# Kernel optimization log

Measured on AMD Instinct MI355X. Metric: run time of the kernel, lower is better.

## Reference

```python
import jax, jax.numpy as jnp
import numpy as np

TEMPERATURE = 0.07
EPS = 1e-12  # matches F.normalize eps

def _l2norm(x, axis):
    n = jnp.sqrt(jnp.sum(x * x, axis=axis, keepdims=True))
    return x / jnp.maximum(n, EPS)

def setup_inputs() -> dict:
    key = jax.random.key(0)
    features = jax.random.normal(key, (512, 256), dtype=jnp.float32)
    return {"features": features}

def reference(features) -> jnp.ndarray:
    B = features.shape[0]
    f = _l2norm(features, axis=1)                      # [B, D]
    fi = f[:, None, :]                                 # broadcast over j
    fj = f[None, :, :]                                 # broadcast over i
    mutual = fi * fj                                   # [B, B, D]
    gate_i = fi * mutual
    gate_j = fj * mutual
    # torch broadcasting: + features adds f[j, k] along trailing dims
    feats_self_i = _l2norm(fi * gate_i + f, axis=2)
    feats_other_i = _l2norm(fi * gate_j + f, axis=2)
    feats_other_j = _l2norm(fj * gate_i + f, axis=2)
    # note: features_self_j is computed in the original but never used in any dot product

    raw_self_i = jnp.einsum('ik,ijk->ij', f, feats_self_i) / TEMPERATURE
    raw_self_j = jnp.einsum('ik,ijk->ij', f, feats_other_j) / TEMPERATURE  # (original uses other_j here)
    raw_other_i = jnp.einsum('ik,ijk->ij', f, feats_other_i) / TEMPERATURE
    raw_other_j = jnp.einsum('ik,ijk->ij', f, feats_other_j) / TEMPERATURE

    logits_mask = 1.0 - jnp.eye(B, dtype=f.dtype)      # zero out diagonal
    exp_sum = (jnp.exp(raw_self_i) + jnp.exp(raw_self_j)
               + jnp.exp(raw_other_i) + jnp.exp(raw_other_j)) * logits_mask
    vs_all = jnp.sum(exp_sum, axis=1, keepdims=True)   # [B, 1]

    log_prob = raw_self_i - jnp.log(vs_all)            # [B, B]
    mean_log_prob_pos = jnp.sum(log_prob, axis=1) / B
    loss = -jnp.mean(mean_log_prob_pos)
    return loss
```

## Files before the change

### kernel.cpp

```cpp
#include <hip/hip_runtime.h>
#include <math.h>

#define Bq 512
#define Dq 256
#define RPB 16
#define PBLK (Bq / RPB)

__device__ __forceinline__ float waveReduceSum(float v) {
    #pragma unroll
    for (int off = 32; off > 0; off >>= 1)
        v += __shfl_xor(v, off, 64);
    return v;
}

__global__ __launch_bounds__(256) void prep_kernel(
        const float* __restrict__ feat,
        float* __restrict__ fT, float* __restrict__ A1,
        float* __restrict__ A2, float* __restrict__ C0,
        float* __restrict__ acc, unsigned int* __restrict__ cnt) {
    const int t = threadIdx.x;
    const int r0 = blockIdx.x * RPB;
    __shared__ float sm[RPB][Dq + 1];
    __shared__ float wpart[RPB][4];
    __shared__ float sinv[RPB];

    float x[RPB];
    #pragma unroll
    for (int r = 0; r < RPB; ++r) x[r] = feat[(r0 + r) * Dq + t];

    const int wid = t >> 6, lane = t & 63;
    #pragma unroll
    for (int r = 0; r < RPB; ++r) {
        float ss = waveReduceSum(x[r] * x[r]);
        if (lane == 0) wpart[r][wid] = ss;
    }
    __syncthreads();
    if (t < RPB) {
        float tot = wpart[t][0] + wpart[t][1] + wpart[t][2] + wpart[t][3];
        sinv[t] = 1.0f / fmaxf(sqrtf(tot), 1e-12f);
    }
    __syncthreads();

    #pragma unroll
    for (int r = 0; r < RPB; ++r) {
        float a  = x[r] * sinv[r];
        float a2 = a * a;
        float c0 = 1.0f + a2 * a;
        A1[(r0 + r) * Dq + t] = a;
        A2[(r0 + r) * Dq + t] = a2;
        C0[(r0 + r) * Dq + t] = c0;
        sm[r][t] = a;
    }
    __syncthreads();

    const int rr = t & 15, kb = t >> 4;
    #pragma unroll
    for (int p = 0; p < 16; ++p) {
        int k = p * 16 + kb;
        fT[k * Bq + r0 + rr] = sm[rr][k];
    }

    if (blockIdx.x == 0 && t == 0) { *acc = 0.0f; *cnt = 0u; }
}

__global__ __launch_bounds__(256) void pair_kernel(
        const float* __restrict__ fT,
        const float* __restrict__ A1, const float* __restrict__ A2,
        const float* __restrict__ C0,
        float* __restrict__ acc, unsigned int* __restrict__ cnt,
        float* __restrict__ out) {
    const int i = blockIdx.x;
    const int t = threadIdx.x;
    const int j0 = 2 * t;

    __shared__ __align__(16) float s_a[Dq];
    __shared__ __align__(16) float s_a2[Dq];
    __shared__ __align__(16) float s_c0[Dq];
    s_a[t]  = A1[i * Dq + t];
    s_a2[t] = A2[i * Dq + t];
    s_c0[t] = C0[i * Dq + t];
    __syncthreads();

    const float4* __restrict__ va  = (const float4*)s_a;
    const float4* __restrict__ va2 = (const float4*)s_a2;
    const float4* __restrict__ vc0 = (const float4*)s_c0;
    const float* __restrict__ pb = fT + j0;

    float du0 = 0.f, nu0 = 0.f, dv0 = 0.f, nv0 = 0.f;
    float du1 = 0.f, nu1 = 0.f, dv1 = 0.f, nv1 = 0.f;

    #pragma unroll 4
    for (int k4 = 0; k4 < Dq / 4; ++k4) {
        float4 a4  = va[k4];
        float4 q4  = va2[k4];
        float4 c4  = vc0[k4];
        const float aa[4] = {a4.x, a4.y, a4.z, a4.w};
        const float qq[4] = {q4.x, q4.y, q4.z, q4.w};
        const float cc[4] = {c4.x, c4.y, c4.z, c4.w};
        #pragma unroll
        for (int kk = 0; kk < 4; ++kk) {
            int k = k4 * 4 + kk;
            float2 bv = *(const float2*)(pb + k * Bq);
            {
                float b  = bv.x;
                float bb = b * b;
                float g  = cc[kk] * b;
                float wb = fmaf(qq[kk], bb, b);
                du0 = fmaf(aa[kk], g,  du0);
                nu0 = fmaf(g,      g,  nu0);
                dv0 = fmaf(aa[kk], wb, dv0);
                nv0 = fmaf(wb,     wb, nv0);
            }
            {
                float b  = bv.y;
                float bb = b * b;
                float g  = cc[kk] * b;
                float wb = fmaf(qq[kk], bb, b);
                du1 = fmaf(aa[kk], g,  du1);
                nu1 = fmaf(g,      g,  nu1);
                dv1 = fmaf(aa[kk], wb, dv1);
                nv1 = fmaf(wb,     wb, nv1);
            }
        }
    }

    const float Tinv = 1.0f / 0.07f;
    float raw_s0 = du0 / fmaxf(sqrtf(nu0), 1e-12f) * Tinv;
    float raw_o0 = dv0 / fmaxf(sqrtf(nv0), 1e-12f) * Tinv;
    float raw_s1 = du1 / fmaxf(sqrtf(nu1), 1e-12f) * Tinv;
    float raw_o1 = dv1 / fmaxf(sqrtf(nv1), 1e-12f) * Tinv;

    float sS = raw_s0 + raw_s1;
    float sV = 0.f;
    if (j0 != i)     sV += expf(raw_s0) + 3.0f * expf(raw_o0);
    if (j0 + 1 != i) sV += expf(raw_s1) + 3.0f * expf(raw_o1);

    sS = waveReduceSum(sS);
    sV = waveReduceSum(sV);
    __shared__ float redS[4], redV[4];
    const int wid = t >> 6, lane = t & 63;
    if (lane == 0) { redS[wid] = sS; redV[wid] = sV; }
    __syncthreads();
    if (t == 0) {
        float S = redS[0] + redS[1] + redS[2] + redS[3];
        float V = redV[0] + redV[1] + redV[2] + redV[3];
        float ti = S * (1.0f / Bq) - logf(V);
        atomicAdd(acc, ti);
        __threadfence();
        unsigned int old = atomicAdd(cnt, 1u);
        if (old == Bq - 1) {
            float tot = atomicAdd(acc, 0.0f);
            out[0] = -tot / (float)Bq;
        }
    }
}

extern "C" void kernel_launch(void* const* d_in, const int* in_sizes, int n_in,
                              void* d_out, int out_size, void* d_ws, size_t ws_size,
                              hipStream_t stream) {
    const float* feat = (const float*)d_in[0];
    float* ws = (float*)d_ws;
    float* fT = ws;
    float* A1 = fT + (size_t)Bq * Dq;
    float* A2 = A1 + (size_t)Bq * Dq;
    float* C0 = A2 + (size_t)Bq * Dq;
    float* acc = C0 + (size_t)Bq * Dq;
    unsigned int* cnt = (unsigned int*)(acc + 1);

    prep_kernel<<<PBLK, 256, 0, stream>>>(feat, fT, A1, A2, C0, acc, cnt);
    pair_kernel<<<Bq, 256, 0, stream>>>(fT, A1, A2, C0, acc, cnt, (float*)d_out);
}
```

Baseline: 91.19 us.

## Tile pair kernel as 2 rows by 256 columns and replace atomics with final reduce

Each pair block now handles two i rows against a 256-wide half of j, so each loaded fT element is reused for two rows instead of loading a float2 for one row. Row normalization and the per-row constants are recomputed inside the pair kernel, which drops the A1/A2/C0 global buffers from the prep kernel. The atomic accumulate with its completion counter is replaced by per-block partial sums written to workspace and a third single-block kernel that does the final reduction. This adds a kernel launch and redundant normalization work per block in exchange for less global traffic and no atomics.

```diff
diff --git a/kernel.cpp b/kernel.cpp
--- a/kernel.cpp
+++ b/kernel.cpp
@@ -14,10 +14,7 @@
 }
 
 __global__ __launch_bounds__(256) void prep_kernel(
-        const float* __restrict__ feat,
-        float* __restrict__ fT, float* __restrict__ A1,
-        float* __restrict__ A2, float* __restrict__ C0,
-        float* __restrict__ acc, unsigned int* __restrict__ cnt) {
+        const float* __restrict__ feat, float* __restrict__ fT) {
     const int t = threadIdx.x;
     const int r0 = blockIdx.x * RPB;
     __shared__ float sm[RPB][Dq + 1];
@@ -40,17 +37,8 @@
         sinv[t] = 1.0f / fmaxf(sqrtf(tot), 1e-12f);
     }
     __syncthreads();
-
     #pragma unroll
-    for (int r = 0; r < RPB; ++r) {
-        float a  = x[r] * sinv[r];
-        float a2 = a * a;
-        float c0 = 1.0f + a2 * a;
-        A1[(r0 + r) * Dq + t] = a;
-        A2[(r0 + r) * Dq + t] = a2;
-        C0[(r0 + r) * Dq + t] = c0;
-        sm[r][t] = a;
-    }
+    for (int r = 0; r < RPB; ++r) sm[r][t] = x[r] * sinv[r];
     __syncthreads();
 
     const int rr = t & 15, kb = t >> 4;
@@ -59,67 +47,75 @@
         int k = p * 16 + kb;
         fT[k * Bq + r0 + rr] = sm[rr][k];
     }
-
-    if (blockIdx.x == 0 && t == 0) { *acc = 0.0f; *cnt = 0u; }
 }
 
 __global__ __launch_bounds__(256) void pair_kernel(
-        const float* __restrict__ fT,
-        const float* __restrict__ A1, const float* __restrict__ A2,
-        const float* __restrict__ C0,
-        float* __restrict__ acc, unsigned int* __restrict__ cnt,
-        float* __restrict__ out) {
-    const int i = blockIdx.x;
+        const float* __restrict__ feat, const float* __restrict__ fT,
+        float* __restrict__ Sp, float* __restrict__ Vp) {
+    const int p = blockIdx.x >> 1;
+    const int h = blockIdx.x & 1;
+    const int i0 = p * 2;
     const int t = threadIdx.x;
-    const int j0 = 2 * t;
+    const int j = h * 256 + t;
+    const int wid = t >> 6, lane = t & 63;
 
-    __shared__ __align__(16) float s_a[Dq];
-    __shared__ __align__(16) float s_a2[Dq];
-    __shared__ __align__(16) float s_c0[Dq];
-    s_a[t]  = A1[i * Dq + t];
-    s_a2[t] = A2[i * Dq + t];
-    s_c0[t] = C0[i * Dq + t];
+    __shared__ __align__(16) float s_a[2][Dq];
+    __shared__ __align__(16) float s_q[2][Dq];
+    __shared__ __align__(16) float s_c[2][Dq];
+    __shared__ float wpart[2][4];
+
+    float x0 = feat[i0 * Dq + t];
+    float x1 = feat[(i0 + 1) * Dq + t];
+    float ss0 = waveReduceSum(x0 * x0);
+    float ss1 = waveReduceSum(x1 * x1);
+    if (lane == 0) { wpart[0][wid] = ss0; wpart[1][wid] = ss1; }
     __syncthreads();
-
-    const float4* __restrict__ va  = (const float4*)s_a;
-    const float4* __restrict__ va2 = (const float4*)s_a2;
-    const float4* __restrict__ vc0 = (const float4*)s_c0;
-    const float* __restrict__ pb = fT + j0;
+    float inv0 = 1.0f / fmaxf(sqrtf(wpart[0][0] + wpart[0][1] + wpart[0][2] + wpart[0][3]), 1e-12f);
+    float inv1 = 1.0f / fmaxf(sqrtf(wpart[1][0] + wpart[1][1] + wpart[1][2] + wpart[1][3]), 1e-12f);
+    {
+        float a0 = x0 * inv0, a1 = x1 * inv1;
+        s_a[0][t] = a0; s_q[0][t] = a0 * a0; s_c[0][t] = 1.0f + a0 * a0 * a0;
+        s_a[1][t] = a1; s_q[1][t] = a1 * a1; s_c[1][t] = 1.0f + a1 * a1 * a1;
+    }
+    __syncthreads();
 
     float du0 = 0.f, nu0 = 0.f, dv0 = 0.f, nv0 = 0.f;
     float du1 = 0.f, nu1 = 0.f, dv1 = 0.f, nv1 = 0.f;
+    const float* __restrict__ pb = fT + j;
 
     #pragma unroll 4
     for (int k4 = 0; k4 < Dq / 4; ++k4) {
-        float4 a4  = va[k4];
-        float4 q4  = va2[k4];
-        float4 c4  = vc0[k4];
-        const float aa[4] = {a4.x, a4.y, a4.z, a4.w};
-        const float qq[4] = {q4.x, q4.y, q4.z, q4.w};
-        const float cc[4] = {c4.x, c4.y, c4.z, c4.w};
+        float4 A0 = ((const float4*)s_a[0])[k4];
+        float4 Q0 = ((const float4*)s_q[0])[k4];
+        float4 Cc0 = ((const float4*)s_c[0])[k4];
+        float4 A1v = ((const float4*)s_a[1])[k4];
+        float4 Q1 = ((const float4*)s_q[1])[k4];
+        float4 Cc1 = ((const float4*)s_c[1])[k4];
         #pragma unroll
         for (int kk = 0; kk < 4; ++kk) {
-            int k = k4 * 4 + kk;
-            float2 bv = *(const float2*)(pb + k * Bq);
+            float b  = pb[(k4 * 4 + kk) * Bq];
+            float bb = b * b;
             {
-                float b  = bv.x;
-                float bb = b * b;
-                float g  = cc[kk] * b;
-                float wb = fmaf(qq[kk], bb, b);
-                du0 = fmaf(aa[kk], g,  du0);
-                nu0 = fmaf(g,      g,  nu0);
-                dv0 = fmaf(aa[kk], wb, dv0);
-                nv0 = fmaf(wb,     wb, nv0);
+                float a = ((const float*)&A0)[kk];
+                float q = ((const float*)&Q0)[kk];
+                float c = ((const float*)&Cc0)[kk];
+                float g  = c * b;
+                float wb = fmaf(q, bb, b);
+                du0 = fmaf(a,  g,  du0);
+                nu0 = fmaf(g,  g,  nu0);
+                dv0 = fmaf(a,  wb, dv0);
+                nv0 = fmaf(wb, wb, nv0);
             }
             {
-                float b  = bv.y;
-                float bb = b * b;
-                float g  = cc[kk] * b;
-                float wb = fmaf(qq[kk], bb, b);
-                du1 = fmaf(aa[kk], g,  du1);
-                nu1 = fmaf(g,      g,  nu1);
-                dv1 = fmaf(aa[kk], wb, dv1);
-                nv1 = fmaf(wb,     wb, nv1);
+                float a = ((const float*)&A1v)[kk];
+                float q = ((const float*)&Q1)[kk];
+                float c = ((const float*)&Cc1)[kk];
+                float g  = c * b;
+                float wb = fmaf(q, bb, b);
+                du1 = fmaf(a,  g,  du1);
+                nu1 = fmaf(g,  g,  nu1);
+                dv1 = fmaf(a,  wb, dv1);
+                nv1 = fmaf(wb, wb, nv1);
             }
         }
     }
@@ -130,28 +126,43 @@
     float raw_s1 = du1 / fmaxf(sqrtf(nu1), 1e-12f) * Tinv;
     float raw_o1 = dv1 / fmaxf(sqrtf(nv1), 1e-12f) * Tinv;
 
-    float sS = raw_s0 + raw_s1;
-    float sV = 0.f;
-    if (j0 != i)     sV += expf(raw_s0) + 3.0f * expf(raw_o0);
-    if (j0 + 1 != i) sV += expf(raw_s1) + 3.0f * expf(raw_o1);
+    float sS0 = raw_s0, sS1 = raw_s1;
+    float sV0 = (j != i0)     ? expf(raw_s0) + 3.0f * expf(raw_o0) : 0.0f;
+    float sV1 = (j != i0 + 1) ? expf(raw_s1) + 3.0f * expf(raw_o1) : 0.0f;
 
-    sS = waveReduceSum(sS);
-    sV = waveReduceSum(sV);
-    __shared__ float redS[4], redV[4];
-    const int wid = t >> 6, lane = t & 63;
-    if (lane == 0) { redS[wid] = sS; redV[wid] = sV; }
+    sS0 = waveReduceSum(sS0); sV0 = waveReduceSum(sV0);
+    sS1 = waveReduceSum(sS1); sV1 = waveReduceSum(sV1);
+    __shared__ float redS[2][4], redV[2][4];
+    if (lane == 0) {
+        redS[0][wid] = sS0; redV[0][wid] = sV0;
+        redS[1][wid] = sS1; redV[1][wid] = sV1;
+    }
     __syncthreads();
-    if (t == 0) {
-        float S = redS[0] + redS[1] + redS[2] + redS[3];
-        float V = redV[0] + redV[1] + redV[2] + redV[3];
-        float ti = S * (1.0f / Bq) - logf(V);
-        atomicAdd(acc, ti);
-        __threadfence();
-        unsigned int old = atomicAdd(cnt, 1u);
-        if (old == Bq - 1) {
-            float tot = atomicAdd(acc, 0.0f);
-            out[0] = -tot / (float)Bq;
-        }
+    if (t < 2) {
+        float S = redS[t][0] + redS[t][1] + redS[t][2] + redS[t][3];
+        float V = redV[t][0] + redV[t][1] + redV[t][2] + redV[t][3];
+        Sp[(i0 + t) * 2 + h] = S;
+        Vp[(i0 + t) * 2 + h] = V;
+    }
+}
+
+__global__ __launch_bounds__(512) void final_kernel(
+        const float* __restrict__ Sp, const float* __restrict__ Vp,
+        float* __restrict__ out) {
+    int i = threadIdx.x;
+    float S = Sp[i * 2] + Sp[i * 2 + 1];
+    float V = Vp[i * 2] + Vp[i * 2 + 1];
+    float t = S * (1.0f / Bq) - logf(V);
+    t = waveReduceSum(t);
+    __shared__ float red[8];
+    int wid = i >> 6, lane = i & 63;
+    if (lane == 0) red[wid] = t;
+    __syncthreads();
+    if (i == 0) {
+        float s = 0.f;
+        #pragma unroll
+        for (int w = 0; w < 8; ++w) s += red[w];
+        out[0] = -s / (float)Bq;
     }
 }
 
@@ -161,12 +172,10 @@
     const float* feat = (const float*)d_in[0];
     float* ws = (float*)d_ws;
     float* fT = ws;
-    float* A1 = fT + (size_t)Bq * Dq;
-    float* A2 = A1 + (size_t)Bq * Dq;
-    float* C0 = A2 + (size_t)Bq * Dq;
-    float* acc = C0 + (size_t)Bq * Dq;
-    unsigned int* cnt = (unsigned int*)(acc + 1);
+    float* Sp = fT + (size_t)Dq * Bq;
+    float* Vp = Sp + (size_t)Bq * 2;
 
-    prep_kernel<<<PBLK, 256, 0, stream>>>(feat, fT, A1, A2, C0, acc, cnt);
-    pair_kernel<<<Bq, 256, 0, stream>>>(fT, A1, A2, C0, acc, cnt, (float*)d_out);
+    prep_kernel<<<PBLK, 256, 0, stream>>>(feat, fT);
+    pair_kernel<<<Bq, 256, 0, stream>>>(feat, fT, Sp, Vp);
+    final_kernel<<<1, Bq, 0, stream>>>(Sp, Vp, (float*)d_out);
 }
```

Result: faster. 78.57 us (-13.8%).
